# Optimization experiments

Measured on AMD Instinct MI355X. Metric: run time of the kernel, lower is better.

The kernel has to match this reference:

```python
import jax, jax.numpy as jnp
import numpy as np

NEG_INF = -1e9  # matches torch masked_fill_(-1000000000.0)


def setup_inputs() -> dict:
    key = jax.random.key(0)
    k1, k2, k3, k4 = jax.random.split(key, 4)
    N, T, D, V = 64, 2048, 256, 256
    query = jax.random.normal(k1, (N, D), dtype=jnp.float32)
    key_t = jax.random.normal(k2, (N, T, D), dtype=jnp.float32)
    value = jax.random.normal(k3, (N, T, V), dtype=jnp.float32)
    lens = jax.random.randint(k4, (N,), 1, T + 1, dtype=jnp.int32)
    return {"query": query, "key": key_t, "value": value, "lens": lens}


def reference(query, key, value, lens):
    # energy: (N, T) = bmm(key (N,T,D), query (N,D,1)).squeeze
    energy = jnp.einsum("ntd,nd->nt", key, query)
    T = energy.shape[1]
    mask = jnp.arange(T)[None, :] >= lens[:, None]  # (N, T) True where padded
    energy = jnp.where(mask, NEG_INF, energy)
    attention = jax.nn.softmax(energy, axis=1)  # (N, T)
    context = jnp.einsum("nt,ntv->nv", attention, value)  # (N, V)
    return (context, attention)
```

## Files before the change

kernel.cpp:

```cpp
#include <hip/hip_runtime.h>
#include <math.h>

#define NEG_INF -1e9f

__global__ __launch_bounds__(256) void energy_kernel(
    const float* __restrict__ query,
    const float* __restrict__ key,
    const int*   __restrict__ lens,
    float*       __restrict__ energy,
    int N, int T)
{
    const int D = 256;
    const int ROWS_PER_WAVE = 8;
    int wave = (int)((blockIdx.x * blockDim.x + threadIdx.x) >> 6);
    int lane = threadIdx.x & 63;
    long long r0 = (long long)wave * ROWS_PER_WAVE;
    int n  = (int)(r0 / T);
    int t0 = (int)(r0 % T);
    if (n >= N) return;

    const float4 q = *reinterpret_cast<const float4*>(query + (long long)n * D + lane * 4);
    const int len = lens[n];
    const float* krow = key + ((long long)n * T + t0) * D + lane * 4;
    float* erow = energy + (long long)n * T + t0;

    #pragma unroll
    for (int i = 0; i < ROWS_PER_WAVE; ++i) {
        const float4 k4 = *reinterpret_cast<const float4*>(krow + (long long)i * D);
        float p = k4.x * q.x + k4.y * q.y + k4.z * q.z + k4.w * q.w;
        #pragma unroll
        for (int off = 32; off >= 1; off >>= 1)
            p += __shfl_xor(p, off, 64);
        if (lane == 0) {
            int t = t0 + i;
            erow[i] = (t >= len) ? NEG_INF : p;
        }
    }
}

__global__ __launch_bounds__(256) void softmax_kernel(
    float* __restrict__ att,
    int T)
{
    __shared__ float sred[256];
    const int n   = blockIdx.x;
    const int tid = threadIdx.x;
    float* row = att + (long long)n * T;

    float vals[8];
    float m = -INFINITY;
    #pragma unroll
    for (int i = 0; i < 8; ++i) {
        vals[i] = row[tid + (i << 8)];
        m = fmaxf(m, vals[i]);
    }
    sred[tid] = m;
    __syncthreads();
    #pragma unroll
    for (int s = 128; s >= 1; s >>= 1) {
        if (tid < s) sred[tid] = fmaxf(sred[tid], sred[tid + s]);
        __syncthreads();
    }
    m = sred[0];
    __syncthreads();

    float sum = 0.f;
    #pragma unroll
    for (int i = 0; i < 8; ++i) {
        vals[i] = __expf(vals[i] - m);
        sum += vals[i];
    }
    sred[tid] = sum;
    __syncthreads();
    #pragma unroll
    for (int s = 128; s >= 1; s >>= 1) {
        if (tid < s) sred[tid] += sred[tid + s];
        __syncthreads();
    }
    const float inv = 1.0f / sred[0];
    #pragma unroll
    for (int i = 0; i < 8; ++i)
        row[tid + (i << 8)] = vals[i] * inv;
}

__global__ __launch_bounds__(256) void context_kernel(
    const float* __restrict__ att,
    const float* __restrict__ value,
    float*       __restrict__ context,
    int T)
{
    const int V = 256;
    const int CHUNK = 128;
    __shared__ float red[4][256];

    const int n    = blockIdx.y;
    const int t0   = blockIdx.x * CHUNK;
    const int wid  = threadIdx.x >> 6;
    const int lane = threadIdx.x & 63;
    const int v4   = lane * 4;

    const float* arow = att + (long long)n * T;
    const float* vbase = value + ((long long)n * T + t0 + wid * 32) * V + v4;

    float4 acc = make_float4(0.f, 0.f, 0.f, 0.f);
    #pragma unroll 4
    for (int i = 0; i < 32; ++i) {
        const float a = arow[t0 + wid * 32 + i];
        const float4 val = *reinterpret_cast<const float4*>(vbase + (long long)i * V);
        acc.x += a * val.x;
        acc.y += a * val.y;
        acc.z += a * val.z;
        acc.w += a * val.w;
    }
    *reinterpret_cast<float4*>(&red[wid][v4]) = acc;
    __syncthreads();

    const int v = threadIdx.x;
    const float s = red[0][v] + red[1][v] + red[2][v] + red[3][v];
    atomicAdd(context + (long long)n * V + v, s);
}

extern "C" void kernel_launch(void* const* d_in, const int* in_sizes, int n_in,
                              void* d_out, int out_size, void* d_ws, size_t ws_size,
                              hipStream_t stream) {
    const float* query = (const float*)d_in[0];
    const float* key   = (const float*)d_in[1];
    const float* value = (const float*)d_in[2];
    const int*   lens  = (const int*)d_in[3];

    const int N = in_sizes[3];
    const int D = in_sizes[0] / N;
    const int T = in_sizes[1] / (N * D);
    const int V = in_sizes[2] / (N * T);
    (void)D; (void)V; (void)d_ws; (void)ws_size; (void)n_in; (void)out_size;

    float* context = (float*)d_out;
    float* att     = (float*)d_out + (long long)N * V;

    hipMemsetAsync(context, 0, (size_t)N * V * sizeof(float), stream);

    {
        long long rows = (long long)N * T;
        long long waves = rows / 8;
        int blocks = (int)((waves + 3) / 4);
        energy_kernel<<<blocks, 256, 0, stream>>>(query, key, lens, att, N, T);
    }
    softmax_kernel<<<N, 256, 0, stream>>>(att, T);
    {
        dim3 grid(T / 128, N);
        context_kernel<<<grid, 256, 0, stream>>>(att, value, context, T);
    }
}
```

Baseline: 282.5 us.

## Skip key/value loads for padded timesteps beyond each sequence length

The energy kernel now splits each wave into four 16-lane groups that each reduce a full 256-wide row. Waves or rows past lens[n] skip the key loads and write the mask value directly. The context kernel returns early for chunks beyond the sequence length and clips its loop to the valid rows. Padded positions have zero attention weight, so this avoids reading the roughly half of key and value memory that is padding. In exchange it adds per-row branching and a variable loop bound.

New measurement: 266.7 us. 5.6% less time.

```diff
diff --git a/kernel.cpp b/kernel.cpp
--- a/kernel.cpp
+++ b/kernel.cpp
@@ -8,33 +8,58 @@
     const float* __restrict__ key,
     const int*   __restrict__ lens,
     float*       __restrict__ energy,
-    int N, int T)
+    int T)
 {
     const int D = 256;
-    const int ROWS_PER_WAVE = 8;
-    int wave = (int)((blockIdx.x * blockDim.x + threadIdx.x) >> 6);
-    int lane = threadIdx.x & 63;
-    long long r0 = (long long)wave * ROWS_PER_WAVE;
-    int n  = (int)(r0 / T);
-    int t0 = (int)(r0 % T);
-    if (n >= N) return;
+    const int ROWS = 16;
+    const int wave = (int)((blockIdx.x * blockDim.x + threadIdx.x) >> 6);
+    const int lane = threadIdx.x & 63;
+    const int g    = lane >> 4;
+    const int sub  = lane & 15;
+    const int wavesPerN = T / ROWS;
+    const int n    = wave / wavesPerN;
+    const int base = (wave % wavesPerN) * ROWS;
 
-    const float4 q = *reinterpret_cast<const float4*>(query + (long long)n * D + lane * 4);
     const int len = lens[n];
-    const float* krow = key + ((long long)n * T + t0) * D + lane * 4;
-    float* erow = energy + (long long)n * T + t0;
+    float* erow = energy + (long long)n * T;
+
+    if (base >= len) {
+        if (sub == 0) {
+            #pragma unroll
+            for (int rq = 0; rq < 4; ++rq)
+                erow[base + rq * 4 + g] = NEG_INF;
+        }
+        return;
+    }
+
+    const float* qn = query + (long long)n * D;
+    const float4 q0 = *reinterpret_cast<const float4*>(qn + sub * 4);
+    const float4 q1 = *reinterpret_cast<const float4*>(qn + sub * 4 + 64);
+    const float4 q2 = *reinterpret_cast<const float4*>(qn + sub * 4 + 128);
+    const float4 q3 = *reinterpret_cast<const float4*>(qn + sub * 4 + 192);
 
     #pragma unroll
-    for (int i = 0; i < ROWS_PER_WAVE; ++i) {
-        const float4 k4 = *reinterpret_cast<const float4*>(krow + (long long)i * D);
-        float p = k4.x * q.x + k4.y * q.y + k4.z * q.z + k4.w * q.w;
-        #pragma unroll
-        for (int off = 32; off >= 1; off >>= 1)
-            p += __shfl_xor(p, off, 64);
-        if (lane == 0) {
-            int t = t0 + i;
-            erow[i] = (t >= len) ? NEG_INF : p;
+    for (int rq = 0; rq < 4; ++rq) {
+        const int row = base + rq * 4 + g;
+        const bool act = row < len;
+        float p = 0.f;
+        if (act) {
+            const float* kr = key + ((long long)n * T + row) * D + sub * 4;
+            const float4 a = *reinterpret_cast<const float4*>(kr);
+            const float4 b = *reinterpret_cast<const float4*>(kr + 64);
+            const float4 c = *reinterpret_cast<const float4*>(kr + 128);
+            const float4 d = *reinterpret_cast<const float4*>(kr + 192);
+            p  = a.x*q0.x + a.y*q0.y + a.z*q0.z + a.w*q0.w;
+            p += b.x*q1.x + b.y*q1.y + b.z*q1.z + b.w*q1.w;
+            p += c.x*q2.x + c.y*q2.y + c.z*q2.z + c.w*q2.w;
+            p += d.x*q3.x + d.y*q3.y + d.z*q3.z + d.w*q3.w;
         }
+        p += __shfl_xor(p, 1, 64);
+        p += __shfl_xor(p, 2, 64);
+        p += __shfl_xor(p, 4, 64);
+        p += __shfl_xor(p, 8, 64);
+        if (sub == 0)
+            erow[row] = act ? p : NEG_INF;
     }
 }
 
@@ -86,6 +111,7 @@
 __global__ __launch_bounds__(256) void context_kernel(
     const float* __restrict__ att,
     const float* __restrict__ value,
+    const int*   __restrict__ lens,
     float*       __restrict__ context,
     int T)
 {
@@ -93,19 +119,23 @@
     const int CHUNK = 128;
     __shared__ float red[4][256];
 
-    const int n    = blockIdx.y;
-    const int t0   = blockIdx.x * CHUNK;
+    const int n   = blockIdx.y;
+    const int t0  = blockIdx.x * CHUNK;
+    const int len = lens[n];
+    if (t0 >= len) return;
+
+    const int rows = min(len - t0, CHUNK);
     const int wid  = threadIdx.x >> 6;
     const int lane = threadIdx.x & 63;
     const int v4   = lane * 4;
 
-    const float* arow = att + (long long)n * T;
-    const float* vbase = value + ((long long)n * T + t0 + wid * 32) * V + v4;
+    const float* arow  = att + (long long)n * T + t0;
+    const float* vbase = value + ((long long)n * T + t0) * V + v4;
 
     float4 acc = make_float4(0.f, 0.f, 0.f, 0.f);
-    #pragma unroll 4
-    for (int i = 0; i < 32; ++i) {
-        const float a = arow[t0 + wid * 32 + i];
+    const int iend = min(wid * 32 + 32, rows);
+    for (int i = wid * 32; i < iend; ++i) {
+        const float a = arow[i];
         const float4 val = *reinterpret_cast<const float4*>(vbase + (long long)i * V);
         acc.x += a * val.x;
         acc.y += a * val.y;
@@ -140,14 +170,13 @@
     hipMemsetAsync(context, 0, (size_t)N * V * sizeof(float), stream);
 
     {
-        long long rows = (long long)N * T;
-        long long waves = rows / 8;
+        long long waves = (long long)N * T / 16;
         int blocks = (int)((waves + 3) / 4);
-        energy_kernel<<<blocks, 256, 0, stream>>>(query, key, lens, att, N, T);
+        energy_kernel<<<blocks, 256, 0, stream>>>(query, key, lens, att, T);
     }
     softmax_kernel<<<N, 256, 0, stream>>>(att, T);
     {
         dim3 grid(T / 128, N);
-        context_kernel<<<grid, 256, 0, stream>>>(att, value, context, T);
+        context_kernel<<<grid, 256, 0, stream>>>(att, value, lens, context, T);
     }
 }
```
